# Optimization experiments

Hardware: AMD Instinct MI355X
Metric: run time of the kernel (lower is better)

Reference implementation:

```python
import jax, jax.numpy as jnp
import numpy as np

K = 4  # top-k from init
BN_IS_FOLDED = True  # BatchNorm (eval mode) folded into per-channel scale s and shift t


def tconv(x, W):
    # x: (b, C, v, n); W: (Cout, Cin, 3) temporal conv, kernel (3,1,1), padding (1,0,0), no bias
    return jax.lax.conv_general_dilated(
        x, W[:, :, :, None], window_strides=(1, 1),
        padding=((1, 1), (0, 0)), dimension_numbers=('NCHW', 'OIHW', 'NCHW'))


def gcn_single(xn, src, dst, Wg, bg):
    # PyG GCNConv: add self-loops, symmetric normalization, then scatter-add.
    N = xn.shape[0]
    xl = xn @ Wg  # (N, C)
    loop = jnp.arange(N, dtype=src.dtype)
    s = jnp.concatenate([src, loop])
    d = jnp.concatenate([dst, loop])
    deg = jax.ops.segment_sum(jnp.ones(s.shape[0], dtype=xn.dtype), d, num_segments=N)
    dinv = jnp.where(deg > 0, jax.lax.rsqrt(deg), 0.0)
    norm = dinv[s] * dinv[d]
    out = jax.ops.segment_sum(norm[:, None] * xl[s], d, num_segments=N)
    return out + bg


def setup_inputs() -> dict:
    key = jax.random.key(0)
    ks = jax.random.split(key, 10)
    C = 256
    x = jax.random.normal(ks[0], (512, C, 16, 16), dtype=jnp.float32)
    Wd = jax.random.normal(ks[1], (C, C, 3), dtype=jnp.float32) * 0.02
    s1 = 1.0 + 0.1 * jax.random.normal(ks[2], (C,), dtype=jnp.float32)
    t1 = 0.1 * jax.random.normal(ks[3], (C,), dtype=jnp.float32)
    Wg = jax.random.normal(ks[4], (C, C), dtype=jnp.float32) * 0.02
    bg = 0.01 * jax.random.normal(ks[5], (C,), dtype=jnp.float32)
    Wu = jax.random.normal(ks[6], (C, C, 3), dtype=jnp.float32) * 0.02
    s2 = 1.0 + 0.1 * jax.random.normal(ks[7], (C,), dtype=jnp.float32)
    t2 = 0.1 * jax.random.normal(ks[8], (C,), dtype=jnp.float32)
    return {"x": x, "batch": 4, "Wd": Wd, "s1": s1, "t1": t1,
            "Wg": Wg, "bg": bg, "Wu": Wu, "s2": s2, "t2": t2}


def reference(x, batch, Wd, s1, t1, Wg, bg, Wu, s2, t2):
    tlen, c, h, w = x.shape
    b = batch
    v = tlen // b
    hw = h * w
    # (tlen,c,h,w) -> (b,c,v,h*w)
    x4 = x.reshape(b, v, c, h, w).transpose(0, 2, 1, 3, 4).reshape(b, c, v, hw)
    xd = tconv(x4, Wd) * s1[None, :, None, None] + t1[None, :, None, None]  # down_conv + BN(eval)

    # --- dynamic graph build (no-grad in original) ---
    f = jax.lax.stop_gradient(xd).transpose(0, 2, 3, 1)  # (b, v, hw, c)
    f1, f2 = f[:, :-1], f[:, 1:]                          # (b, t_1, hw, c)
    t_1 = v - 1
    sq1 = jnp.sum(f1 * f1, axis=-1)                       # (b,t_1,hw)
    sq2 = jnp.sum(f2 * f2, axis=-1)
    dots = jnp.einsum('btnc,btmc->btnm', f1, f2)
    d2 = jnp.maximum(sq1[..., :, None] + sq2[..., None, :] - 2.0 * dots, 0.0)
    sim = -jnp.sqrt(d2).reshape(b, t_1, hw * hw)
    sim = sim / jnp.maximum(jnp.linalg.norm(sim, axis=-1, keepdims=True), 1e-12)  # F.normalize
    sim = jnp.where(sim < 0.05, 100.0, sim)
    _, idx = jax.lax.top_k(sim, K)                        # (b, t_1, K)
    frame = jnp.arange(t_1, dtype=jnp.int32)[None, :, None]
    row = (idx // hw).astype(jnp.int32) + frame * hw
    col = (idx % hw).astype(jnp.int32) + (frame + 1) * hw
    row = row.reshape(b, -1)
    col = col.reshape(b, -1)
    src = jnp.concatenate([row, col], axis=1)             # forward + reversed edges
    dst = jnp.concatenate([col, row], axis=1)

    # --- per-sample GCN (batched with vmap) ---
    nodes = xd.transpose(0, 2, 3, 1).reshape(b, v * hw, c)  # 'b c v n -> b (v n) c'
    out = jax.vmap(lambda xn, s, d: gcn_single(xn, s, d, Wg, bg))(nodes, src, dst)

    # --- up path ---
    o4 = out.transpose(0, 2, 1).reshape(b, c, v, hw)
    xu = tconv(o4, Wu) * s2[None, :, None, None] + t2[None, :, None, None]
    return xu.reshape(b, c, v, h, w).transpose(0, 2, 1, 3, 4).reshape(tlen, c, h, w)
```

## Files before the change

kernel.cpp:

```cpp
#include <hip/hip_runtime.h>

typedef __attribute__((ext_vector_type(8))) short short8;
typedef __attribute__((ext_vector_type(4))) float f32x4;
typedef unsigned short u16;
typedef unsigned int u32;

__device__ __forceinline__ void gld_lds16(const void* g, void* l) {
  __builtin_amdgcn_global_load_lds((const __attribute__((address_space(1))) void*)g,
                                   (__attribute__((address_space(3))) void*)l,
                                   16, 0, 0);
}

__device__ __forceinline__ u16 f2b(float x) {
  union { float f; u32 u; } v; v.f = x;
  u32 u = v.u;
  return (u16)((u + 0x7FFFu + ((u >> 16) & 1u)) >> 16);
}
__device__ __forceinline__ float b2f(u16 x) {
  union { u32 u; float f; } v; v.u = ((u32)x) << 16; return v.f;
}
__device__ __forceinline__ u32 pack_pair(float lo, float hi) {
  return (u32)f2b(lo) | ((u32)f2b(hi) << 16);
}

__global__ __launch_bounds__(256) void k_prep(const float* __restrict__ Wd, const float* __restrict__ Wg,
                                              const float* __restrict__ Wu,
                                              const float* __restrict__ s1, const float* __restrict__ t1,
                                              const float* __restrict__ bg,
                                              u16* __restrict__ WdT, u16* __restrict__ Wup,
                                              u16* __restrict__ WgS,
                                              float* __restrict__ c0, float* __restrict__ tWg) {
  int blk = blockIdx.x;
  int tid = threadIdx.x;
  if (blk == 1024) {
    int j = tid;
    float a = 0.f;
    for (int co = 0; co < 256; ++co) a += t1[co] * Wg[co * 256 + j];
    tWg[j] = a;
    c0[j] = a + bg[j];
    return;
  }
  int id = blk * 256 + tid;
  if (id < 196608) {
    int kk = id >> 16;
    int rem = id & 65535;
    int a = rem >> 8, b = rem & 255;
    Wup[id] = f2b(Wu[(u32)a * 768 + (u32)b * 3 + kk]);
    WdT[id] = f2b(Wd[(u32)b * 768 + (u32)a * 3 + kk]);
  } else {
    int id2 = id - 196608;
    int j = id2 >> 8, co = id2 & 255;
    WgS[id2] = f2b(Wg[co * 256 + j] * s1[co]);
  }
}

__global__ __launch_bounds__(256) void k_transpose(const float* __restrict__ x, u16* __restrict__ xT) {
  __shared__ u16 tile[64][72];
  int blk = blockIdx.x;
  int tl = blk >> 4;
  int sub = blk & 15;
  int ci0 = (sub >> 2) << 6;
  int p0 = (sub & 3) << 6;
  int tid = threadIdx.x;
  int i = tid >> 2;
  int ch = tid & 3;
  const float* gsrc = x + (size_t)tl * 65536 + (ci0 + i) * 256 + p0 + ch * 16;
  __align__(16) u16 cv[16];
#pragma unroll
  for (int v4 = 0; v4 < 4; ++v4) {
    float4 f = *(const float4*)(gsrc + v4 * 4);
    cv[v4 * 4 + 0] = f2b(f.x);
    cv[v4 * 4 + 1] = f2b(f.y);
    cv[v4 * 4 + 2] = f2b(f.z);
    cv[v4 * 4 + 3] = f2b(f.w);
  }
  *(uint4*)&tile[i][ch * 16] = *(const uint4*)&cv[0];
  *(uint4*)&tile[i][ch * 16 + 8] = *(const uint4*)&cv[8];
  __syncthreads();
  __align__(16) u16 tmp[16];
#pragma unroll
  for (int cc = 0; cc < 16; ++cc) tmp[cc] = tile[ch * 16 + cc][i];
  u16* gdst = xT + (size_t)tl * 65536 + (p0 + i) * 256 + ci0 + ch * 16;
  *(uint4*)(gdst) = *(const uint4*)&tmp[0];
  *(uint4*)(gdst + 8) = *(const uint4*)&tmp[8];
}

__device__ __forceinline__ void stage_tile(const u16* __restrict__ g, int ldg, u16* s, int w, int lane) {
  int r = lane >> 2;
  int cc = (lane & 3) * 8;
#pragma unroll
  for (int j = 0; j < 2; ++j) {
    gld_lds16(g + (w * 32 + j * 16 + r) * ldg + cc, s + (w * 32 + j * 16) * 32);
  }
}

__device__ __forceinline__ void mfma_tiles(const u16* sA, const u16* sB, f32x4 acc[4][4],
                                           int wr, int wc, int lane) {
  int m16 = lane & 15;
  int q8 = (lane >> 4) * 8;
  short8 a[4], b[4];
#pragma unroll
  for (int mi = 0; mi < 4; ++mi) a[mi] = *(const short8*)(sA + (wr * 64 + mi * 16 + m16) * 32 + q8);
#pragma unroll
  for (int ni = 0; ni < 4; ++ni) b[ni] = *(const short8*)(sB + (wc * 64 + ni * 16 + m16) * 32 + q8);
#pragma unroll
  for (int mi = 0; mi < 4; ++mi)
#pragma unroll
    for (int ni = 0; ni < 4; ++ni)
      acc[mi][ni] = __builtin_amdgcn_mfma_f32_16x16x32_bf16(a[mi], b[ni], acc[mi][ni], 0, 0, 0);
}

__device__ __forceinline__ void store_pairs(u16* base, int row0, int stride, int colb,
                                            const float v[4], bool ev) {
  float pv[4];
#pragma unroll
  for (int r = 0; r < 4; ++r) pv[r] = __shfl_xor(v[r], 1, 64);
  u32 wd0 = ev ? pack_pair(v[0], pv[0]) : pack_pair(pv[0], v[0]);
  u32 wd1 = ev ? pack_pair(v[1], pv[1]) : pack_pair(pv[1], v[1]);
  u32 wd2 = ev ? pack_pair(v[2], pv[2]) : pack_pair(pv[2], v[2]);
  u32 wd3 = ev ? pack_pair(v[3], pv[3]) : pack_pair(pv[3], v[3]);
  u32 wa = ev ? wd0 : wd2;
  u32 wb = ev ? wd1 : wd3;
  int rs = ev ? 0 : 2;
  *(u32*)(base + (size_t)(row0 + rs) * stride + colb) = wa;
  *(u32*)(base + (size_t)(row0 + rs + 1) * stride + colb) = wb;
}

__device__ __forceinline__ void store_pairs_f32(float* base, int row0, int stride, int colb,
                                                const float v[4], bool ev) {
  float pv[4];
#pragma unroll
  for (int r = 0; r < 4; ++r) pv[r] = __shfl_xor(v[r], 1, 64);
  float2 wa, wb;
  if (ev) { wa = make_float2(v[0], pv[0]); wb = make_float2(v[1], pv[1]); }
  else    { wa = make_float2(pv[2], v[2]); wb = make_float2(pv[3], v[3]); }
  int rs = ev ? 0 : 2;
  *(float2*)(base + (size_t)(row0 + rs) * stride + colb) = wa;
  *(float2*)(base + (size_t)(row0 + rs + 1) * stride + colb) = wb;
}

__global__ __launch_bounds__(256) void k_wcomb(const u16* __restrict__ WgS, const u16* __restrict__ WdT,
                                               u16* __restrict__ Wcomb) {
  __shared__ u16 sA[128 * 32];
  __shared__ u16 sB[128 * 32];
  int blk = blockIdx.x;
  int kk = blk >> 2;
  int tile = blk & 3;
  int tm = tile >> 1, tn = tile & 1;
  int tid = threadIdx.x, lane = tid & 63, w = tid >> 6;
  int wr = w >> 1, wc = w & 1;
  f32x4 acc[4][4];
#pragma unroll
  for (int i = 0; i < 4; ++i)
#pragma unroll
    for (int j = 0; j < 4; ++j) acc[i][j] = (f32x4){0.f, 0.f, 0.f, 0.f};
  const u16* gA = WgS + (size_t)(tm * 128) * 256;
  const u16* gB = WdT + (size_t)kk * 65536 + (size_t)(tn * 128) * 256;
  for (int ks = 0; ks < 8; ++ks) {
    stage_tile(gA + ks * 32, 256, sA, w, lane);
    stage_tile(gB + ks * 32, 256, sB, w, lane);
    __syncthreads();
    mfma_tiles(sA, sB, acc, wr, wc, lane);
    __syncthreads();
  }
  int q = lane >> 4, c = lane & 15;
  bool ev = (lane & 1) == 0;
  u16* obase = Wcomb + (size_t)kk * 65536;
#pragma unroll
  for (int mi = 0; mi < 4; ++mi) {
    int row0 = tm * 128 + wr * 64 + mi * 16 + q * 4;
#pragma unroll
    for (int ni = 0; ni < 4; ++ni) {
      float v[4];
#pragma unroll
      for (int r = 0; r < 4; ++r) v[r] = acc[mi][ni][r];
      int colb = tn * 128 + wc * 64 + ni * 16 + (c & ~1);
      store_pairs(obase, row0, 256, colb, v, ev);
    }
  }
}

__global__ __launch_bounds__(256) void k_g12(const u16* __restrict__ xT, const u16* __restrict__ Wcomb,
                                             const float* __restrict__ c0, const float* __restrict__ tWg,
                                             u16* __restrict__ outp, float* __restrict__ edge) {
  __shared__ u16 sA[128 * 64];
  __shared__ u16 sB[128 * 64];
  int blk = blockIdx.x;
  int bt = blk >> 2;
  int tile = blk & 3;
  int tm = tile >> 1, tn = tile & 1;
  int t = bt & 127;
  int tid = threadIdx.x, lane = tid & 63, w = tid >> 6;
  int wr = w >> 1, wc = w & 1;
  f32x4 acc[4][4];
#pragma unroll
  for (int i = 0; i < 4; ++i)
#pragma unroll
    for (int j = 0; j < 4; ++j) acc[i][j] = (f32x4){0.f, 0.f, 0.f, 0.f};

#pragma unroll
  for (int kk = 0; kk < 3; ++kk) {
    int tp = t - 1 + kk;
    if (tp < 0 || tp > 127) continue;
    const u16* gA = xT + ((size_t)(bt - t + tp) * 256 + tm * 128) * 256;
    const u16* gB = Wcomb + (size_t)kk * 65536 + (size_t)(tn * 128) * 256;
    for (int ks = 0; ks < 4; ++ks) {
      stage_tile(gA + ks * 64, 256, sA, w, lane);
      stage_tile(gA + ks * 64 + 32, 256, sA + 4096, w, lane);
      stage_tile(gB + ks * 64, 256, sB, w, lane);
      stage_tile(gB + ks * 64 + 32, 256, sB + 4096, w, lane);
      __syncthreads();
      mfma_tiles(sA, sB, acc, wr, wc, lane);
      mfma_tiles(sA + 4096, sB + 4096, acc, wr, wc, lane);
      __syncthreads();
    }
  }
  int q = lane >> 4, c = lane & 15;
  bool ev = (lane & 1) == 0;
  float c0v[4], tWgv[4];
#pragma unroll
  for (int ni = 0; ni < 4; ++ni) {
    int j = tn * 128 + wc * 64 + ni * 16 + c;
    c0v[ni] = c0[j];
    tWgv[ni] = tWg[j];
  }
  bool eblk = (tm == 0) && (wr == 0) && (q == 0);
  u16* obase = outp + (size_t)bt * 65536;
#pragma unroll
  for (int mi = 0; mi < 4; ++mi) {
    int row0 = tm * 128 + wr * 64 + mi * 16 + q * 4;
#pragma unroll
    for (int ni = 0; ni < 4; ++ni) {
      float v[4];
#pragma unroll
      for (int r = 0; r < 4; ++r) v[r] = acc[mi][ni][r] + c0v[ni];
      int colb = tn * 128 + wc * 64 + ni * 16 + (c & ~1);
      store_pairs(obase, row0, 256, colb, v, ev);
      if (eblk && mi == 0) {
        float vE[4];
#pragma unroll
        for (int r = 0; r < 4; ++r) vE[r] = acc[0][ni][r] + tWgv[ni];
        store_pairs_f32(edge + (size_t)bt * 1024, 0, 256, colb, vE, ev);
      }
    }
  }
}

__device__ __forceinline__ float dinv0(int t) {
  if (t == 0) return 0.44721359549995793f;
  if (t == 127) return 0.7071067811865476f;
  return 0.4082482904638631f;
}
__global__ __launch_bounds__(256) void k_fix(const float* __restrict__ edge, const float* __restrict__ bg,
                                             u16* __restrict__ outp) {
  int bt = blockIdx.x;
  int t = bt & 127;
  int j = threadIdx.x;
  const float ISQ2 = 0.7071067811865476f;
  float bgv = bg[j];
  float e_t = edge[(size_t)bt * 1024 + j];
  float At = dinv0(t);
  float o0 = bgv + At * At * e_t;
  if (t <= 126) {
    float At1 = dinv0(t + 1);
    const float* en = edge + (size_t)(bt + 1) * 1024;
    float s = At1 * en[j] + ISQ2 * (en[256 + j] + en[512 + j] + en[768 + j]);
    o0 += At * s;
  }
  float em1 = 0.f, Atm1 = 0.f;
  if (t >= 1) {
    Atm1 = dinv0(t - 1);
    em1 = edge[(size_t)(bt - 1) * 1024 + j];
    o0 += At * Atm1 * em1;
  }
  u16* ob = outp + (size_t)bt * 65536;
  ob[j] = f2b(o0);
#pragma unroll
  for (int k = 1; k <= 3; ++k) {
    float m = edge[(size_t)bt * 1024 + k * 256 + j];
    float ok = (t == 0) ? (bgv + m) : (bgv + 0.5f * m + ISQ2 * Atm1 * em1);
    ob[k * 256 + j] = f2b(ok);
  }
}

__global__ __launch_bounds__(256) void k_g3(const u16* __restrict__ outp, const u16* __restrict__ Wup,
                                            const float* __restrict__ s2, const float* __restrict__ t2,
                                            float* __restrict__ y) {
  __shared__ u16 sA[128 * 64];
  __shared__ u16 sB[128 * 64];
  __shared__ float ss2[128], st2[128];
  int blk = blockIdx.x;
  int bt = blk >> 2;
  int tile = blk & 3;
  int tm = tile >> 1, tn = tile & 1;
  int t = bt & 127;
  int tid = threadIdx.x, lane = tid & 63, w = tid >> 6;
  int wr = w >> 1, wc = w & 1;
  if (tid < 128) {
    int co = tm * 128 + tid;
    ss2[tid] = s2[co];
    st2[tid] = t2[co];
  }
  f32x4 acc[4][4];
#pragma unroll
  for (int i = 0; i < 4; ++i)
#pragma unroll
    for (int j = 0; j < 4; ++j) acc[i][j] = (f32x4){0.f, 0.f, 0.f, 0.f};

#pragma unroll
  for (int kk = 0; kk < 3; ++kk) {
    int tp = t - 1 + kk;
    if (tp < 0 || tp > 127) continue;
    const u16* gA = Wup + (size_t)kk * 65536 + (size_t)(tm * 128) * 256;
    const u16* gB = outp + ((size_t)(bt - t + tp) * 256 + tn * 128) * 256;
    for (int ks = 0; ks < 4; ++ks) {
      stage_tile(gA + ks * 64, 256, sA, w, lane);
      stage_tile(gA + ks * 64 + 32, 256, sA + 4096, w, lane);
      stage_tile(gB + ks * 64, 256, sB, w, lane);
      stage_tile(gB + ks * 64 + 32, 256, sB + 4096, w, lane);
      __syncthreads();
      mfma_tiles(sA, sB, acc, wr, wc, lane);
      mfma_tiles(sA + 4096, sB + 4096, acc, wr, wc, lane);
      __syncthreads();
    }
  }
  int q = lane >> 4, c = lane & 15;
  bool ev = (lane & 1) == 0;
  float* ybase = y + (size_t)bt * 65536;
#pragma unroll
  for (int mi = 0; mi < 4; ++mi) {
    int rl = wr * 64 + mi * 16 + q * 4;
    float sv[4], tv[4];
#pragma unroll
    for (int r = 0; r < 4; ++r) { sv[r] = ss2[rl + r]; tv[r] = st2[rl + r]; }
#pragma unroll
    for (int ni = 0; ni < 4; ++ni) {
      float v[4];
#pragma unroll
      for (int r = 0; r < 4; ++r) v[r] = acc[mi][ni][r] * sv[r] + tv[r];
      int colb = tn * 128 + wc * 64 + ni * 16 + (c & ~1);
      store_pairs_f32(ybase, tm * 128 + rl, 256, colb, v, ev);
    }
  }
}

extern "C" void kernel_launch(void* const* d_in, const int* in_sizes, int n_in,
                              void* d_out, int out_size, void* d_ws, size_t ws_size,
                              hipStream_t stream) {
  (void)in_sizes; (void)n_in; (void)out_size; (void)ws_size;
  const float* x  = (const float*)d_in[0];
  const float* Wd = (const float*)d_in[2];
  const float* s1 = (const float*)d_in[3];
  const float* t1 = (const float*)d_in[4];
  const float* Wg = (const float*)d_in[5];
  const float* bg = (const float*)d_in[6];
  const float* Wu = (const float*)d_in[7];
  const float* s2 = (const float*)d_in[8];
  const float* t2 = (const float*)d_in[9];
  float* y = (float*)d_out;
  char* ws = (char*)d_ws;
  u16*   outp  = (u16*)(ws);
  u16*   xT    = (u16*)(ws + 67108864);
  float* edge  = (float*)(ws + 134217728);
  u16*   WdT   = (u16*)(ws + 134217728);
  u16*   WgS   = (u16*)(ws + 134611072);
  u16*   Wup   = (u16*)(ws + 136314880);
  u16*   Wcomb = (u16*)(ws + 136708096);
  float* c0    = (float*)(ws + 137101312);
  float* tWg   = (float*)(ws + 137102336);

  k_prep<<<dim3(1025), dim3(256), 0, stream>>>(Wd, Wg, Wu, s1, t1, bg, WdT, Wup, WgS, c0, tWg);
  k_wcomb<<<dim3(12), dim3(256), 0, stream>>>(WgS, WdT, Wcomb);
  k_transpose<<<dim3(8192), dim3(256), 0, stream>>>(x, xT);
  k_g12<<<dim3(2048), dim3(256), 0, stream>>>(xT, Wcomb, c0, tWg, outp, edge);
  k_fix<<<dim3(512), dim3(256), 0, stream>>>(edge, bg, outp);
  k_g3<<<dim3(2048), dim3(256), 0, stream>>>(outp, Wup, s2, t2, y);
}
```

Measured before the change: 429.2 us.

## Double-buffer LDS staging in GEMM kernels and swizzle block order

Both the k_g12 and k_g3 GEMM kernels now use double-buffered 32-wide K chunks in shared memory. Each iteration issues the async global-to-LDS loads for the next chunk before running the MFMAs on the current one, which halves the barriers per chunk and overlaps loads with compute. Block indices are also remapped with an XCD-style stride-8 swizzle, so neighbouring logical tiles that share operands land on the same chiplet's L2. The cost is smaller K chunks, which means more iterations, and it depends on the async LDS loads being correctly ordered by the single barrier.

```diff
diff --git a/kernel.cpp b/kernel.cpp
--- a/kernel.cpp
+++ b/kernel.cpp
@@ -183,11 +183,12 @@
 __global__ __launch_bounds__(256) void k_g12(const u16* __restrict__ xT, const u16* __restrict__ Wcomb,
                                              const float* __restrict__ c0, const float* __restrict__ tWg,
                                              u16* __restrict__ outp, float* __restrict__ edge) {
-  __shared__ u16 sA[128 * 64];
-  __shared__ u16 sB[128 * 64];
-  int blk = blockIdx.x;
-  int bt = blk >> 2;
-  int tile = blk & 3;
+  __shared__ u16 sA[2][128 * 32];
+  __shared__ u16 sB[2][128 * 32];
+  int b = blockIdx.x;
+  int logical = (b & 7) * 256 + (b >> 3);
+  int bt = logical >> 2;
+  int tile = logical & 3;
   int tm = tile >> 1, tn = tile & 1;
   int t = bt & 127;
   int tid = threadIdx.x, lane = tid & 63, w = tid >> 6;
@@ -198,29 +199,37 @@
 #pragma unroll
     for (int j = 0; j < 4; ++j) acc[i][j] = (f32x4){0.f, 0.f, 0.f, 0.f};
 
+  const u16* Ap[3];
+  const u16* Bp[3];
+  int nf = 0;
 #pragma unroll
   for (int kk = 0; kk < 3; ++kk) {
     int tp = t - 1 + kk;
     if (tp < 0 || tp > 127) continue;
-    const u16* gA = xT + ((size_t)(bt - t + tp) * 256 + tm * 128) * 256;
-    const u16* gB = Wcomb + (size_t)kk * 65536 + (size_t)(tn * 128) * 256;
-    for (int ks = 0; ks < 4; ++ks) {
-      stage_tile(gA + ks * 64, 256, sA, w, lane);
-      stage_tile(gA + ks * 64 + 32, 256, sA + 4096, w, lane);
-      stage_tile(gB + ks * 64, 256, sB, w, lane);
-      stage_tile(gB + ks * 64 + 32, 256, sB + 4096, w, lane);
-      __syncthreads();
-      mfma_tiles(sA, sB, acc, wr, wc, lane);
-      mfma_tiles(sA + 4096, sB + 4096, acc, wr, wc, lane);
-      __syncthreads();
-    }
-  }
-  int q = lane >> 4, c = lane & 15;
+    Ap[nf] = xT + ((size_t)(bt - t + tp) * 256 + tm * 128) * 256;
+    Bp[nf] = Wcomb + (size_t)kk * 65536 + (size_t)(tn * 128) * 256;
+    ++nf;
+  }
+  int nc = nf * 8;
+  stage_tile(Ap[0], 256, sA[0], w, lane);
+  stage_tile(Bp[0], 256, sB[0], w, lane);
+  __syncthreads();
+  for (int c = 0; c < nc; ++c) {
+    int nx = c + 1;
+    if (nx < nc) {
+      stage_tile(Ap[nx >> 3] + (nx & 7) * 32, 256, sA[nx & 1], w, lane);
+      stage_tile(Bp[nx >> 3] + (nx & 7) * 32, 256, sB[nx & 1], w, lane);
+    }
+    mfma_tiles(sA[c & 1], sB[c & 1], acc, wr, wc, lane);
+    __syncthreads();
+  }
+
+  int q = lane >> 4, cc16 = lane & 15;
   bool ev = (lane & 1) == 0;
   float c0v[4], tWgv[4];
 #pragma unroll
   for (int ni = 0; ni < 4; ++ni) {
-    int j = tn * 128 + wc * 64 + ni * 16 + c;
+    int j = tn * 128 + wc * 64 + ni * 16 + cc16;
     c0v[ni] = c0[j];
     tWgv[ni] = tWg[j];
   }
@@ -234,7 +243,7 @@
       float v[4];
 #pragma unroll
       for (int r = 0; r < 4; ++r) v[r] = acc[mi][ni][r] + c0v[ni];
-      int colb = tn * 128 + wc * 64 + ni * 16 + (c & ~1);
+      int colb = tn * 128 + wc * 64 + ni * 16 + (cc16 & ~1);
       store_pairs(obase, row0, 256, colb, v, ev);
       if (eblk && mi == 0) {
         float vE[4];
@@ -286,12 +295,13 @@
 __global__ __launch_bounds__(256) void k_g3(const u16* __restrict__ outp, const u16* __restrict__ Wup,
                                             const float* __restrict__ s2, const float* __restrict__ t2,
                                             float* __restrict__ y) {
-  __shared__ u16 sA[128 * 64];
-  __shared__ u16 sB[128 * 64];
+  __shared__ u16 sA[2][128 * 32];
+  __shared__ u16 sB[2][128 * 32];
   __shared__ float ss2[128], st2[128];
-  int blk = blockIdx.x;
-  int bt = blk >> 2;
-  int tile = blk & 3;
+  int b = blockIdx.x;
+  int logical = (b & 7) * 256 + (b >> 3);
+  int bt = logical >> 2;
+  int tile = logical & 3;
   int tm = tile >> 1, tn = tile & 1;
   int t = bt & 127;
   int tid = threadIdx.x, lane = tid & 63, w = tid >> 6;
@@ -307,24 +317,32 @@
 #pragma unroll
     for (int j = 0; j < 4; ++j) acc[i][j] = (f32x4){0.f, 0.f, 0.f, 0.f};
 
+  const u16* Ap[3];
+  const u16* Bp[3];
+  int nf = 0;
 #pragma unroll
   for (int kk = 0; kk < 3; ++kk) {
     int tp = t - 1 + kk;
     if (tp < 0 || tp > 127) continue;
-    const u16* gA = Wup + (size_t)kk * 65536 + (size_t)(tm * 128) * 256;
-    const u16* gB = outp + ((size_t)(bt - t + tp) * 256 + tn * 128) * 256;
-    for (int ks = 0; ks < 4; ++ks) {
-      stage_tile(gA + ks * 64, 256, sA, w, lane);
-      stage_tile(gA + ks * 64 + 32, 256, sA + 4096, w, lane);
-      stage_tile(gB + ks * 64, 256, sB, w, lane);
-      stage_tile(gB + ks * 64 + 32, 256, sB + 4096, w, lane);
-      __syncthreads();
-      mfma_tiles(sA, sB, acc, wr, wc, lane);
-      mfma_tiles(sA + 4096, sB + 4096, acc, wr, wc, lane);
-      __syncthreads();
-    }
-  }
-  int q = lane >> 4, c = lane & 15;
+    Ap[nf] = Wup + (size_t)kk * 65536 + (size_t)(tm * 128) * 256;
+    Bp[nf] = outp + ((size_t)(bt - t + tp) * 256 + tn * 128) * 256;
+    ++nf;
+  }
+  int nc = nf * 8;
+  stage_tile(Ap[0], 256, sA[0], w, lane);
+  stage_tile(Bp[0], 256, sB[0], w, lane);
+  __syncthreads();
+  for (int c = 0; c < nc; ++c) {
+    int nx = c + 1;
+    if (nx < nc) {
+      stage_tile(Ap[nx >> 3] + (nx & 7) * 32, 256, sA[nx & 1], w, lane);
+      stage_tile(Bp[nx >> 3] + (nx & 7) * 32, 256, sB[nx & 1], w, lane);
+    }
+    mfma_tiles(sA[c & 1], sB[c & 1], acc, wr, wc, lane);
+    __syncthreads();
+  }
+
+  int q = lane >> 4, cc16 = lane & 15;
   bool ev = (lane & 1) == 0;
   float* ybase = y + (size_t)bt * 65536;
 #pragma unroll
@@ -338,7 +356,7 @@
       float v[4];
 #pragma unroll
       for (int r = 0; r < 4; ++r) v[r] = acc[mi][ni][r] * sv[r] + tv[r];
-      int colb = tn * 128 + wc * 64 + ni * 16 + (c & ~1);
+      int colb = tn * 128 + wc * 64 + ni * 16 + (cc16 & ~1);
       store_pairs_f32(ybase, tm * 128 + rl, 256, colb, v, ev);
     }
   }
```

New measurement: 421.5 us. About the same (-1.8%).
